# Kernel tuning notes

Measured on AMD Instinct MI355X. Metric: run time of the kernel, lower is better.

Reference implementation:

```python
import jax, jax.numpy as jnp
import numpy as np

NEG_INF = -1e9  # torch code uses masked_fill with -1e9, not -inf


def setup_inputs() -> dict:
    key = jax.random.key(0)
    ks = jax.random.split(key, 6)
    B, S, WL, D1, D2, OUT = 32, 128, 20, 300, 300, 300
    sequence = jax.random.normal(ks[0], (B, S, WL, D1), dtype=jnp.float32)
    vector = jax.random.normal(ks[1], (B, S, D2), dtype=jnp.float32)
    char_masks = jax.random.randint(ks[2], (B, S, WL), 0, 2, dtype=jnp.int32)
    W = jax.random.normal(ks[3], (OUT, D1 + D2), dtype=jnp.float32) * (1.0 / np.sqrt(D1 + D2))
    b = jax.random.normal(ks[4], (OUT,), dtype=jnp.float32) * 0.01
    v = jax.random.uniform(ks[5], (OUT,), dtype=jnp.float32, minval=-0.01, maxval=0.01)
    return {"sequence": sequence, "vector": vector, "char_masks": char_masks,
            "W": W, "b": b, "v": v}


def reference(sequence, vector, char_masks, W, b, v):
    # sequence: (B,S,WL,D1); vector: (B,S,D2); char_masks: (B,S,WL)
    D1 = sequence.shape[-1]
    # Linear on concat([sequence, vector_expanded]) == split matmul (avoids
    # materializing the (B,S,WL,D1+D2) concat):
    Ws, Wv = W[:, :D1], W[:, D1:]
    lin = (jnp.einsum('bswd,od->bswo', sequence, Ws)
           + jnp.einsum('bsd,od->bso', vector, Wv)[:, :, None, :]
           + b)                       # (B,S,WL,OUT)
    score = jnp.einsum('bswo,o->bsw', jnp.tanh(lin), v)  # (B,S,WL)
    score = jnp.where(char_masks == 0, NEG_INF, score)
    alphas = jax.nn.softmax(score, axis=2)               # over word_len
    weighted = jnp.einsum('bsw,bswd->bsd', alphas, sequence)  # (B,S,D1)
    return weighted
```

## Files before the change

### kernel.cpp

```cpp
#include <hip/hip_runtime.h>
#include <math.h>

#define NEG_INF -1000000000.0f

#define WL_  20
#define D1_  300
#define D2_  300
#define OUT_ 300
#define BS_  4096
#define PPB  2
#define NBLK (BS_ / PPB)
#define BM   40
#define MT   3
#define KS   10
#define FR   512
#define SLABS (MT * KS)

typedef __attribute__((ext_vector_type(8))) short bf16x8;
typedef __attribute__((ext_vector_type(8))) short short8v;
typedef __attribute__((ext_vector_type(4))) float f32x4;
typedef __attribute__((ext_vector_type(4))) unsigned int uint4v;

__device__ short g_Bpk[KS * 20 * FR];
__device__ short g_Wvpk[KS * 20 * FR];
__device__ float g_vlin[(size_t)BS_ * 320];

__device__ inline short f2bf(float f) {
    unsigned u = __float_as_uint(f);
    u += 0x7FFFu + ((u >> 16) & 1u);
    return (short)(u >> 16);
}
__device__ inline float bf2f(short s) {
    return __uint_as_float(((unsigned)(unsigned short)s) << 16);
}

__device__ inline void pack_store(short* Am, int s, int lane, float4 fa, float4 fb) {
    unsigned u0 = __float_as_uint(fa.x) + 0x8000u;
    unsigned u1 = __float_as_uint(fa.y) + 0x8000u;
    unsigned u2 = __float_as_uint(fa.z) + 0x8000u;
    unsigned u3 = __float_as_uint(fa.w) + 0x8000u;
    unsigned u4 = __float_as_uint(fb.x) + 0x8000u;
    unsigned u5 = __float_as_uint(fb.y) + 0x8000u;
    unsigned u6 = __float_as_uint(fb.z) + 0x8000u;
    unsigned u7 = __float_as_uint(fb.w) + 0x8000u;
    uint4v w;
    w.x = __builtin_amdgcn_perm(u1, u0, 0x07060302u);
    w.y = __builtin_amdgcn_perm(u3, u2, 0x07060302u);
    w.z = __builtin_amdgcn_perm(u5, u4, 0x07060302u);
    w.w = __builtin_amdgcn_perm(u7, u6, 0x07060302u);
    *(uint4v*)(Am + ((size_t)s * 64 + lane) * 8) = w;
}

#define GB (KS * 20 * 64)
#define GT2 (GB + GB)

__global__ __launch_bounds__(256) void prep_small(
    const float* __restrict__ W, const float* __restrict__ bias,
    short* Bpk, short* Wvpk)
{
    if (!Bpk) { Bpk = g_Bpk; Wvpk = g_Wvpk; }
    const int id = blockIdx.x * 256 + threadIdx.x;
    if (id >= GT2) return;
    short8v o8 = {0, 0, 0, 0, 0, 0, 0, 0};
    if (id < GB) {
        const int lane = id & 63, g = id >> 6;
        const int q = lane >> 4, l15 = lane & 15;
        const int ks = g / 20, tile = g % 20;
        const int o = tile * 16 + l15, k0 = ks * 32 + q * 8;
        if (o < OUT_) {
            #pragma unroll
            for (int e = 0; e < 8; ++e) {
                const int k = k0 + e;
                if (k < D1_) o8[e] = f2bf(W[(size_t)o * (D1_ + D2_) + k]);
            }
        }
        *(short8v*)(Bpk + (size_t)id * 8) = o8;
    } else {
        const int id4 = id - GB;
        const int lane = id4 & 63, g = id4 >> 6;
        const int q = lane >> 4, l15 = lane & 15;
        const int ks = g / 20, tile = g % 20;
        const int o = tile * 16 + l15, k0 = ks * 32 + q * 8;
        if (o < OUT_) {
            #pragma unroll
            for (int e = 0; e < 8; ++e) {
                const int k = k0 + e;
                if (k < D2_)        o8[e] = f2bf(W[(size_t)o * (D1_ + D2_) + D1_ + k]);
                else if (k == 319)  o8[e] = f2bf(bias[o]);
            }
        }
        *(short8v*)(Wvpk + (size_t)id4 * 8) = o8;
    }
}

__global__ __launch_bounds__(256) void vlin_direct(
    const float* __restrict__ vec, const short* Wvpk, float* vlin)
{
    if (!Wvpk) { Wvpk = g_Wvpk; vlin = g_vlin; }
    const int mtile = blockIdx.x;
    const int tid  = threadIdx.x;
    const int lane = tid & 63;
    const int wv   = tid >> 6;
    const int q = lane >> 4, l15 = lane & 15;

    const float* vp = vec + (size_t)(mtile * 16 + l15) * D2_;
    float4 ra[KS], rb[KS];
    #pragma unroll
    for (int ks = 0; ks < KS; ++ks) {
        const int k0 = ks * 32 + q * 8;
        float4 fa = {0.f, 0.f, 0.f, 0.f}, fb = {0.f, 0.f, 0.f, 0.f};
        if (k0 < 296) { fa = *(const float4*)(vp + k0); fb = *(const float4*)(vp + k0 + 4); }
        else if (k0 == 296) { fa = *(const float4*)(vp + k0); }
        ra[ks] = fa; rb[ks] = fb;
    }
    bf16x8 frag[KS];
    #pragma unroll
    for (int ks = 0; ks < KS; ++ks) {
        const int k0 = ks * 32 + q * 8;
        const float f[8] = {ra[ks].x, ra[ks].y, ra[ks].z, ra[ks].w,
                            rb[ks].x, rb[ks].y, rb[ks].z, rb[ks].w};
        short8v av = {0, 0, 0, 0, 0, 0, 0, 0};
        #pragma unroll
        for (int e = 0; e < 8; ++e) {
            const int k = k0 + e;
            if (k < D2_)       av[e] = f2bf(f[e]);
            else if (k == 319) av[e] = (short)0x3F80;
        }
        frag[ks] = (bf16x8)av;
    }

    f32x4 acc[5];
    #pragma unroll
    for (int j = 0; j < 5; ++j) acc[j] = {0.f, 0.f, 0.f, 0.f};
    const short* pwb = Wvpk + (size_t)(wv * 5) * FR + lane * 8;
    #pragma unroll
    for (int ks = 0; ks < KS; ++ks) {
        #pragma unroll
        for (int j = 0; j < 5; ++j) {
            const bf16x8 b = *(const bf16x8*)(pwb + j * FR);
            acc[j] = __builtin_amdgcn_mfma_f32_16x16x32_bf16(frag[ks], b, acc[j], 0, 0, 0);
        }
        pwb += 20 * FR;
    }
    const int row0 = mtile * 16 + q * 4;
    #pragma unroll
    for (int j = 0; j < 5; ++j)
        #pragma unroll
        for (int r = 0; r < 4; ++r)
            vlin[(size_t)(row0 + r) * 320 + (wv * 5 + j) * 16 + l15] = acc[j][r];
}

__global__ __launch_bounds__(256, 2) void attn_fused(
    const float* __restrict__ seq,
    const int*   __restrict__ masks,
    const float* __restrict__ vvec,
    const short* Bpk,
    const float* vlinbuf,
    float*       __restrict__ out)
{
    if (!Bpk) { Bpk = g_Bpk; vlinbuf = g_vlin; }

    __shared__ short Am[MT * KS * FR];
    __shared__ float sp[4][BM];
    __shared__ float alpha_lds[BM];

    const int tid  = threadIdx.x;
    const int lane = tid & 63;
    const int wv   = tid >> 6;
    const int q    = lane >> 4;
    const int l15  = lane & 15;
    const int blk  = blockIdx.x;

    {
        const float* sbase = seq + (size_t)blk * BM * D1_;
        float4 ra[8], rb[8];
        #pragma unroll
        for (int it = 0; it < 8; ++it) {
            const int s = wv + it * 4;
            float4 fa = {0.f, 0.f, 0.f, 0.f}, fb = {0.f, 0.f, 0.f, 0.f};
            if (s < SLABS) {
                const int tile = s / KS, ks = s % KS;
                const int row = tile * 16 + l15;
                const int k0 = ks * 32 + q * 8;
                if (row < BM) {
                    const float* p = sbase + (size_t)row * D1_ + k0;
                    if (k0 < 296) { fa = *(const float4*)p; fb = *(const float4*)(p + 4); }
                    else if (k0 == 296) { fa = *(const float4*)p; }
                }
            }
            ra[it] = fa; rb[it] = fb;
        }
        #pragma unroll
        for (int it = 0; it < 8; ++it) {
            const int s = wv + it * 4;
            if (s < SLABS) pack_store(Am, s, lane, ra[it], rb[it]);
        }
    }

    float vj[5];
    #pragma unroll
    for (int j = 0; j < 5; ++j) {
        const int col = wv * 80 + j * 16 + l15;
        vj[j] = (col < OUT_) ? vvec[col] : 0.f;
    }
    float vlp[PPB][5];
    #pragma unroll
    for (int p = 0; p < PPB; ++p)
        #pragma unroll
        for (int j = 0; j < 5; ++j)
            vlp[p][j] = vlinbuf[(size_t)(blk * PPB + p) * 320 + wv * 80 + j * 16 + l15];
    __syncthreads();

    f32x4 acc[MT][5];
    #pragma unroll
    for (int i = 0; i < MT; ++i)
        #pragma unroll
        for (int j = 0; j < 5; ++j) acc[i][j] = {0.f, 0.f, 0.f, 0.f};

    const short* pb[5];
    #pragma unroll
    for (int j = 0; j < 5; ++j)
        pb[j] = Bpk + (size_t)(wv * 5 + j) * FR + lane * 8;

    #pragma unroll
    for (int ks = 0; ks < KS; ++ks) {
        bf16x8 a[MT], b[5];
        #pragma unroll
        for (int i = 0; i < MT; ++i)
            a[i] = *(const bf16x8*)(Am + (((size_t)i * KS + ks) * 64 + lane) * 8);
        #pragma unroll
        for (int j = 0; j < 5; ++j)
            b[j] = *(const bf16x8*)(pb[j] + (size_t)ks * 20 * FR);
        #pragma unroll
        for (int i = 0; i < MT; ++i)
            #pragma unroll
            for (int j = 0; j < 5; ++j)
                acc[i][j] = __builtin_amdgcn_mfma_f32_16x16x32_bf16(a[i], b[j], acc[i][j], 0, 0, 0);
    }

    #pragma unroll
    for (int i = 0; i < MT; ++i) {
        #pragma unroll
        for (int r = 0; r < 4; ++r) {
            const int row = i * 16 + q * 4 + r;
            const bool hi = (row >= 20);
            float s = 0.f;
            #pragma unroll
            for (int j = 0; j < 5; ++j) {
                const float vlv = (i == 0) ? vlp[0][j]
                                : (i == 2) ? vlp[1][j]
                                : (hi ? vlp[1][j] : vlp[0][j]);
                const float x = acc[i][j][r] + vlv;
                const float e = __expf(2.f * x);
                s += (1.f - 2.f / (e + 1.f)) * vj[j];
            }
            s += __shfl_xor(s, 1, 64);
            s += __shfl_xor(s, 2, 64);
            s += __shfl_xor(s, 4, 64);
            s += __shfl_xor(s, 8, 64);
            if (l15 == 0 && row < BM) sp[wv][row] = s;
        }
    }
    __syncthreads();

    if (tid < PPB * 32) {
        const int p = tid >> 5;
        const int w = tid & 31;
        float s;
        if (w < WL_) {
            const int row = p * WL_ + w;
            const float sc = sp[0][row] + sp[1][row] + sp[2][row] + sp[3][row];
            const int mk = masks[(size_t)(blk * PPB + p) * WL_ + w];
            s = (mk == 0) ? NEG_INF : sc;
        } else {
            s = -INFINITY;
        }
        float m = s;
        #pragma unroll
        for (int off = 16; off; off >>= 1)
            m = fmaxf(m, __shfl_xor(m, off, 32));
        const float e = __expf(s - m);
        float sum = e;
        #pragma unroll
        for (int off = 16; off; off >>= 1)
            sum += __shfl_xor(sum, off, 32);
        if (w < WL_) alpha_lds[p * WL_ + w] = e / sum;
    }
    __syncthreads();

    if (tid < PPB * 38) {
        const int p = tid / 38, ch = tid % 38;
        const int ks2 = ch >> 2, q2 = ch & 3;
        const int wst = ch % WL_;
        float o8[8] = {0.f, 0.f, 0.f, 0.f, 0.f, 0.f, 0.f, 0.f};
        #pragma unroll
        for (int wi = 0; wi < WL_; ++wi) {
            int w = wst + wi; if (w >= WL_) w -= WL_;
            const int row = p * WL_ + w;
            const int tl = row >> 4, l = row & 15;
            const bf16x8 s8 = *(const bf16x8*)(Am + (((size_t)tl * KS + ks2) * 64 + q2 * 16 + l) * 8);
            const float a = alpha_lds[row];
            #pragma unroll
            for (int e2 = 0; e2 < 8; ++e2) o8[e2] += a * bf2f(s8[e2]);
        }
        const int d0 = ch * 8, gp = blk * PPB + p;
        float* dst = out + (size_t)gp * OUT_ + d0;
        if (d0 + 8 <= OUT_) {
            *(float4*)dst       = {o8[0], o8[1], o8[2], o8[3]};
            *(float4*)(dst + 4) = {o8[4], o8[5], o8[6], o8[7]};
        } else {
            *(float4*)dst = {o8[0], o8[1], o8[2], o8[3]};
        }
    }
}

extern "C" void kernel_launch(void* const* d_in, const int* in_sizes, int n_in,
                              void* d_out, int out_size, void* d_ws, size_t ws_size,
                              hipStream_t stream) {
    const float* seq   = (const float*)d_in[0];
    const float* vec   = (const float*)d_in[1];
    const int*   masks = (const int*)d_in[2];
    const float* W     = (const float*)d_in[3];
    const float* b     = (const float*)d_in[4];
    const float* v     = (const float*)d_in[5];
    float* out = (float*)d_out;

    constexpr size_t SZ_B = sizeof(short) * (size_t)KS * 20 * FR;
    constexpr size_t SZ_L = sizeof(float) * (size_t)BS_ * 320;
    constexpr size_t NEED = SZ_B * 2 + SZ_L;
    short *Bpk = nullptr, *Wvpk = nullptr;
    float *vlin = nullptr;
    if (d_ws && ws_size >= NEED) {
        char* p = (char*)d_ws;
        Bpk  = (short*)p; p += SZ_B;
        Wvpk = (short*)p; p += SZ_B;
        vlin = (float*)p;
    }

    prep_small<<<(GT2 + 255) / 256, 256, 0, stream>>>(W, b, Bpk, Wvpk);
    vlin_direct<<<256, 256, 0, stream>>>(vec, Wvpk, vlin);
    attn_fused<<<NBLK, 256, 0, stream>>>(seq, masks, v, Bpk, vlin, out);
}
```

Measured before the change: 197.8 us.

## Merge prep and vlin kernels; double-buffer sequence tiles in persistent attention blocks

The weight-packing and vector-linear kernels become one launch: the vlin blocks now read and convert the W2/bias slice straight from global memory instead of waiting on a packed copy. The attention kernel now processes four tiles per block. It double-buffers the packed sequence in LDS and prefetches the next tile's sequence, vlin values and masks into registers while the current tile computes. This aims to hide global load latency and cut one launch. In exchange it doubles LDS use, raises register pressure (which may lower occupancy), and runs a quarter as many blocks.

```diff
diff --git a/kernel.cpp b/kernel.cpp
--- a/kernel.cpp
+++ b/kernel.cpp
@@ -9,7 +9,8 @@
 #define OUT_ 300
 #define BS_  4096
 #define PPB  2
-#define NBLK (BS_ / PPB)
+#define TPB  4
+#define NBLKP (BS_ / (PPB * TPB))
 #define BM   40
 #define MT   3
 #define KS   10
@@ -22,7 +23,6 @@
 typedef __attribute__((ext_vector_type(4))) unsigned int uint4v;
 
 __device__ short g_Bpk[KS * 20 * FR];
-__device__ short g_Wvpk[KS * 20 * FR];
 __device__ float g_vlin[(size_t)BS_ * 320];
 
 __device__ inline short f2bf(float f) {
@@ -34,7 +34,7 @@
     return __uint_as_float(((unsigned)(unsigned short)s) << 16);
 }
 
-__device__ inline void pack_store(short* Am, int s, int lane, float4 fa, float4 fb) {
+__device__ inline void pack_store(short* dst, int s, int lane, float4 fa, float4 fb) {
     unsigned u0 = __float_as_uint(fa.x) + 0x8000u;
     unsigned u1 = __float_as_uint(fa.y) + 0x8000u;
     unsigned u2 = __float_as_uint(fa.z) + 0x8000u;
@@ -48,25 +48,30 @@
     w.y = __builtin_amdgcn_perm(u3, u2, 0x07060302u);
     w.z = __builtin_amdgcn_perm(u5, u4, 0x07060302u);
     w.w = __builtin_amdgcn_perm(u7, u6, 0x07060302u);
-    *(uint4v*)(Am + ((size_t)s * 64 + lane) * 8) = w;
+    *(uint4v*)(dst + ((size_t)s * 64 + lane) * 8) = w;
 }
 
 #define GB (KS * 20 * 64)
-#define GT2 (GB + GB)
-
-__global__ __launch_bounds__(256) void prep_small(
+#define PREP_BLKS ((GB + 255) / 256)
+#define VLIN_BLKS 256
+
+__global__ __launch_bounds__(256) void prep_and_vlin(
     const float* __restrict__ W, const float* __restrict__ bias,
-    short* Bpk, short* Wvpk)
+    const float* __restrict__ vec,
+    short* Bpk, float* vlin)
 {
-    if (!Bpk) { Bpk = g_Bpk; Wvpk = g_Wvpk; }
-    const int id = blockIdx.x * 256 + threadIdx.x;
-    if (id >= GT2) return;
-    short8v o8 = {0, 0, 0, 0, 0, 0, 0, 0};
-    if (id < GB) {
-        const int lane = id & 63, g = id >> 6;
-        const int q = lane >> 4, l15 = lane & 15;
+    if (!Bpk) { Bpk = g_Bpk; vlin = g_vlin; }
+    const int tid  = threadIdx.x;
+    const int lane = tid & 63;
+    const int q = lane >> 4, l15 = lane & 15;
+
+    if (blockIdx.x < PREP_BLKS) {
+        const int id = blockIdx.x * 256 + tid;
+        if (id >= GB) return;
+        const int g = id >> 6;
         const int ks = g / 20, tile = g % 20;
         const int o = tile * 16 + l15, k0 = ks * 32 + q * 8;
+        short8v o8 = {0, 0, 0, 0, 0, 0, 0, 0};
         if (o < OUT_) {
             #pragma unroll
             for (int e = 0; e < 8; ++e) {
@@ -75,33 +80,11 @@
             }
         }
         *(short8v*)(Bpk + (size_t)id * 8) = o8;
-    } else {
-        const int id4 = id - GB;
-        const int lane = id4 & 63, g = id4 >> 6;
-        const int q = lane >> 4, l15 = lane & 15;
-        const int ks = g / 20, tile = g % 20;
-        const int o = tile * 16 + l15, k0 = ks * 32 + q * 8;
-        if (o < OUT_) {
-            #pragma unroll
-            for (int e = 0; e < 8; ++e) {
-                const int k = k0 + e;
-                if (k < D2_)        o8[e] = f2bf(W[(size_t)o * (D1_ + D2_) + D1_ + k]);
-                else if (k == 319)  o8[e] = f2bf(bias[o]);
-            }
-        }
-        *(short8v*)(Wvpk + (size_t)id4 * 8) = o8;
-    }
-}
-
-__global__ __launch_bounds__(256) void vlin_direct(
-    const float* __restrict__ vec, const short* Wvpk, float* vlin)
-{
-    if (!Wvpk) { Wvpk = g_Wvpk; vlin = g_vlin; }
-    const int mtile = blockIdx.x;
-    const int tid  = threadIdx.x;
-    const int lane = tid & 63;
-    const int wv   = tid >> 6;
-    const int q = lane >> 4, l15 = lane & 15;
+        return;
+    }
+
+    const int mtile = blockIdx.x - PREP_BLKS;
+    const int wv = tid >> 6;
 
     const float* vp = vec + (size_t)(mtile * 16 + l15) * D2_;
     float4 ra[KS], rb[KS];
@@ -132,16 +115,46 @@
     f32x4 acc[5];
     #pragma unroll
     for (int j = 0; j < 5; ++j) acc[j] = {0.f, 0.f, 0.f, 0.f};
-    const short* pwb = Wvpk + (size_t)(wv * 5) * FR + lane * 8;
-    #pragma unroll
-    for (int ks = 0; ks < KS; ++ks) {
-        #pragma unroll
-        for (int j = 0; j < 5; ++j) {
-            const bf16x8 b = *(const bf16x8*)(pwb + j * FR);
-            acc[j] = __builtin_amdgcn_mfma_f32_16x16x32_bf16(frag[ks], b, acc[j], 0, 0, 0);
-        }
-        pwb += 20 * FR;
-    }
+
+    #pragma unroll
+    for (int j = 0; j < 5; ++j) {
+        const int jt = wv * 5 + j;
+        const int o = jt * 16 + l15;
+        float4 ba[KS], bb[KS];
+        float bv = 0.f;
+        if (o < OUT_) {
+            const float* wp = W + (size_t)o * (D1_ + D2_) + D1_;
+            #pragma unroll
+            for (int ks = 0; ks < KS; ++ks) {
+                const int k0 = ks * 32 + q * 8;
+                float4 fa = {0.f, 0.f, 0.f, 0.f}, fb = {0.f, 0.f, 0.f, 0.f};
+                if (k0 < 296) { fa = *(const float4*)(wp + k0); fb = *(const float4*)(wp + k0 + 4); }
+                else if (k0 == 296) { fa = *(const float4*)(wp + k0); }
+                ba[ks] = fa; bb[ks] = fb;
+            }
+            bv = bias[o];
+        } else {
+            #pragma unroll
+            for (int ks = 0; ks < KS; ++ks) {
+                ba[ks] = {0.f, 0.f, 0.f, 0.f}; bb[ks] = {0.f, 0.f, 0.f, 0.f};
+            }
+        }
+        #pragma unroll
+        for (int ks = 0; ks < KS; ++ks) {
+            const int k0 = ks * 32 + q * 8;
+            const float f[8] = {ba[ks].x, ba[ks].y, ba[ks].z, ba[ks].w,
+                                bb[ks].x, bb[ks].y, bb[ks].z, bb[ks].w};
+            short8v bvv = {0, 0, 0, 0, 0, 0, 0, 0};
+            #pragma unroll
+            for (int e = 0; e < 8; ++e) {
+                const int k = k0 + e;
+                if (k < D2_)       bvv[e] = f2bf(f[e]);
+                else if (k == 319) bvv[e] = f2bf(bv);
+            }
+            acc[j] = __builtin_amdgcn_mfma_f32_16x16x32_bf16(frag[ks], (bf16x8)bvv, acc[j], 0, 0, 0);
+        }
+    }
+
     const int row0 = mtile * 16 + q * 4;
     #pragma unroll
     for (int j = 0; j < 5; ++j)
@@ -160,7 +173,7 @@
 {
     if (!Bpk) { Bpk = g_Bpk; vlinbuf = g_vlin; }
 
-    __shared__ short Am[MT * KS * FR];
+    __shared__ short Am[2][SLABS * FR];
     __shared__ float sp[4][BM];
     __shared__ float alpha_lds[BM];
 
@@ -170,10 +183,14 @@
     const int q    = lane >> 4;
     const int l15  = lane & 15;
     const int blk  = blockIdx.x;
-
-    {
-        const float* sbase = seq + (size_t)blk * BM * D1_;
-        float4 ra[8], rb[8];
+    const int gt0  = blk * TPB;
+
+    float4 ra[8], rb[8];
+    float vlpc[PPB][5], vlpn[PPB][5];
+    int mkc = 0, mkn = 0;
+
+    auto issue_tile = [&](int gt) {
+        const float* sbase = seq + (size_t)gt * BM * D1_;
         #pragma unroll
         for (int it = 0; it < 8; ++it) {
             const int s = wv + it * 4;
@@ -191,11 +208,22 @@
             ra[it] = fa; rb[it] = fb;
         }
         #pragma unroll
+        for (int p = 0; p < PPB; ++p)
+            #pragma unroll
+            for (int j = 0; j < 5; ++j)
+                vlpn[p][j] = vlinbuf[(size_t)(gt * PPB + p) * 320 + wv * 80 + j * 16 + l15];
+        if (tid < PPB * 32) {
+            const int p = tid >> 5, w = tid & 31;
+            mkn = (w < WL_) ? masks[(size_t)(gt * PPB + p) * WL_ + w] : 0;
+        }
+    };
+    auto pack_tile = [&](short* dst) {
+        #pragma unroll
         for (int it = 0; it < 8; ++it) {
             const int s = wv + it * 4;
-            if (s < SLABS) pack_store(Am, s, lane, ra[it], rb[it]);
-        }
-    }
+            if (s < SLABS) pack_store(dst, s, lane, ra[it], rb[it]);
+        }
+    };
 
     float vj[5];
     #pragma unroll
@@ -203,113 +231,134 @@
         const int col = wv * 80 + j * 16 + l15;
         vj[j] = (col < OUT_) ? vvec[col] : 0.f;
     }
-    float vlp[PPB][5];
+
+    issue_tile(gt0);
+    pack_tile(&Am[0][0]);
     #pragma unroll
     for (int p = 0; p < PPB; ++p)
         #pragma unroll
-        for (int j = 0; j < 5; ++j)
-            vlp[p][j] = vlinbuf[(size_t)(blk * PPB + p) * 320 + wv * 80 + j * 16 + l15];
-    __syncthreads();
-
-    f32x4 acc[MT][5];
-    #pragma unroll
-    for (int i = 0; i < MT; ++i)
-        #pragma unroll
-        for (int j = 0; j < 5; ++j) acc[i][j] = {0.f, 0.f, 0.f, 0.f};
+        for (int j = 0; j < 5; ++j) vlpc[p][j] = vlpn[p][j];
+    mkc = mkn;
+    issue_tile(gt0 + 1);
+
+    short* cur = &Am[0][0];
+    short* nxt = &Am[1][0];
 
     const short* pb[5];
     #pragma unroll
     for (int j = 0; j < 5; ++j)
         pb[j] = Bpk + (size_t)(wv * 5 + j) * FR + lane * 8;
 
-    #pragma unroll
-    for (int ks = 0; ks < KS; ++ks) {
-        bf16x8 a[MT], b[5];
+    #pragma unroll 1
+    for (int t = 0; t < TPB; ++t) {
+        const int gt = gt0 + t;
+        __syncthreads();
+
+        f32x4 acc[MT][5];
         #pragma unroll
         for (int i = 0; i < MT; ++i)
-            a[i] = *(const bf16x8*)(Am + (((size_t)i * KS + ks) * 64 + lane) * 8);
-        #pragma unroll
-        for (int j = 0; j < 5; ++j)
-            b[j] = *(const bf16x8*)(pb[j] + (size_t)ks * 20 * FR);
-        #pragma unroll
-        for (int i = 0; i < MT; ++i)
+            #pragma unroll
+            for (int j = 0; j < 5; ++j) acc[i][j] = {0.f, 0.f, 0.f, 0.f};
+
+        #pragma unroll
+        for (int ks = 0; ks < KS; ++ks) {
+            bf16x8 a[MT], b[5];
+            #pragma unroll
+            for (int i = 0; i < MT; ++i)
+                a[i] = *(const bf16x8*)(cur + (((size_t)i * KS + ks) * 64 + lane) * 8);
             #pragma unroll
             for (int j = 0; j < 5; ++j)
-                acc[i][j] = __builtin_amdgcn_mfma_f32_16x16x32_bf16(a[i], b[j], acc[i][j], 0, 0, 0);
-    }
-
-    #pragma unroll
-    for (int i = 0; i < MT; ++i) {
-        #pragma unroll
-        for (int r = 0; r < 4; ++r) {
-            const int row = i * 16 + q * 4 + r;
-            const bool hi = (row >= 20);
-            float s = 0.f;
-            #pragma unroll
-            for (int j = 0; j < 5; ++j) {
-                const float vlv = (i == 0) ? vlp[0][j]
-                                : (i == 2) ? vlp[1][j]
-                                : (hi ? vlp[1][j] : vlp[0][j]);
-                const float x = acc[i][j][r] + vlv;
-                const float e = __expf(2.f * x);
-                s += (1.f - 2.f / (e + 1.f)) * vj[j];
-            }
-            s += __shfl_xor(s, 1, 64);
-            s += __shfl_xor(s, 2, 64);
-            s += __shfl_xor(s, 4, 64);
-            s += __shfl_xor(s, 8, 64);
-            if (l15 == 0 && row < BM) sp[wv][row] = s;
-        }
-    }
-    __syncthreads();
-
-    if (tid < PPB * 32) {
-        const int p = tid >> 5;
-        const int w = tid & 31;
-        float s;
-        if (w < WL_) {
-            const int row = p * WL_ + w;
-            const float sc = sp[0][row] + sp[1][row] + sp[2][row] + sp[3][row];
-            const int mk = masks[(size_t)(blk * PPB + p) * WL_ + w];
-            s = (mk == 0) ? NEG_INF : sc;
-        } else {
-            s = -INFINITY;
-        }
-        float m = s;
-        #pragma unroll
-        for (int off = 16; off; off >>= 1)
-            m = fmaxf(m, __shfl_xor(m, off, 32));
-        const float e = __expf(s - m);
-        float sum = e;
-        #pragma unroll
-        for (int off = 16; off; off >>= 1)
-            sum += __shfl_xor(sum, off, 32);
-        if (w < WL_) alpha_lds[p * WL_ + w] = e / sum;
-    }
-    __syncthreads();
-
-    if (tid < PPB * 38) {
-        const int p = tid / 38, ch = tid % 38;
-        const int ks2 = ch >> 2, q2 = ch & 3;
-        const int wst = ch % WL_;
-        float o8[8] = {0.f, 0.f, 0.f, 0.f, 0.f, 0.f, 0.f, 0.f};
-        #pragma unroll
-        for (int wi = 0; wi < WL_; ++wi) {
-            int w = wst + wi; if (w >= WL_) w -= WL_;
-            const int row = p * WL_ + w;
-            const int tl = row >> 4, l = row & 15;
-            const bf16x8 s8 = *(const bf16x8*)(Am + (((size_t)tl * KS + ks2) * 64 + q2 * 16 + l) * 8);
-            const float a = alpha_lds[row];
-            #pragma unroll
-            for (int e2 = 0; e2 < 8; ++e2) o8[e2] += a * bf2f(s8[e2]);
-        }
-        const int d0 = ch * 8, gp = blk * PPB + p;
-        float* dst = out + (size_t)gp * OUT_ + d0;
-        if (d0 + 8 <= OUT_) {
-            *(float4*)dst       = {o8[0], o8[1], o8[2], o8[3]};
-            *(float4*)(dst + 4) = {o8[4], o8[5], o8[6], o8[7]};
-        } else {
-            *(float4*)dst = {o8[0], o8[1], o8[2], o8[3]};
+                b[j] = *(const bf16x8*)(pb[j] + (size_t)ks * 20 * FR);
+            #pragma unroll
+            for (int i = 0; i < MT; ++i)
+                #pragma unroll
+                for (int j = 0; j < 5; ++j)
+                    acc[i][j] = __builtin_amdgcn_mfma_f32_16x16x32_bf16(a[i], b[j], acc[i][j], 0, 0, 0);
+        }
+
+        #pragma unroll
+        for (int i = 0; i < MT; ++i) {
+            #pragma unroll
+            for (int r = 0; r < 4; ++r) {
+                const int row = i * 16 + q * 4 + r;
+                const bool hi = (row >= 20);
+                float s = 0.f;
+                #pragma unroll
+                for (int j = 0; j < 5; ++j) {
+                    const float vlv = (i == 0) ? vlpc[0][j]
+                                    : (i == 2) ? vlpc[1][j]
+                                    : (hi ? vlpc[1][j] : vlpc[0][j]);
+                    const float x = acc[i][j][r] + vlv;
+                    const float e = __expf(2.f * x);
+                    s += (1.f - 2.f / (e + 1.f)) * vj[j];
+                }
+                s += __shfl_xor(s, 1, 64);
+                s += __shfl_xor(s, 2, 64);
+                s += __shfl_xor(s, 4, 64);
+                s += __shfl_xor(s, 8, 64);
+                if (l15 == 0 && row < BM) sp[wv][row] = s;
+            }
+        }
+        __syncthreads();
+
+        if (tid < PPB * 32) {
+            const int p = tid >> 5;
+            const int w = tid & 31;
+            float s;
+            if (w < WL_) {
+                const int row = p * WL_ + w;
+                const float sc = sp[0][row] + sp[1][row] + sp[2][row] + sp[3][row];
+                s = (mkc == 0) ? NEG_INF : sc;
+            } else {
+                s = -INFINITY;
+            }
+            float m = s;
+            #pragma unroll
+            for (int off = 16; off; off >>= 1)
+                m = fmaxf(m, __shfl_xor(m, off, 32));
+            const float e = __expf(s - m);
+            float sum = e;
+            #pragma unroll
+            for (int off = 16; off; off >>= 1)
+                sum += __shfl_xor(sum, off, 32);
+            if (w < WL_) alpha_lds[p * WL_ + w] = e / sum;
+        }
+        __syncthreads();
+
+        if (tid < PPB * 38) {
+            const int p = tid / 38, ch = tid % 38;
+            const int ks2 = ch >> 2, q2 = ch & 3;
+            const int wst = ch % WL_;
+            float o8[8] = {0.f, 0.f, 0.f, 0.f, 0.f, 0.f, 0.f, 0.f};
+            #pragma unroll
+            for (int wi = 0; wi < WL_; ++wi) {
+                int w = wst + wi; if (w >= WL_) w -= WL_;
+                const int row = p * WL_ + w;
+                const int tl = row >> 4, l = row & 15;
+                const bf16x8 s8 = *(const bf16x8*)(cur + (((size_t)tl * KS + ks2) * 64 + q2 * 16 + l) * 8);
+                const float a = alpha_lds[row];
+                #pragma unroll
+                for (int e2 = 0; e2 < 8; ++e2) o8[e2] += a * bf2f(s8[e2]);
+            }
+            const int d0 = ch * 8, gp = gt * PPB + p;
+            float* dst = out + (size_t)gp * OUT_ + d0;
+            if (d0 + 8 <= OUT_) {
+                *(float4*)dst       = {o8[0], o8[1], o8[2], o8[3]};
+                *(float4*)(dst + 4) = {o8[4], o8[5], o8[6], o8[7]};
+            } else {
+                *(float4*)dst = {o8[0], o8[1], o8[2], o8[3]};
+            }
+        }
+
+        if (t + 1 < TPB) {
+            pack_tile(nxt);
+            #pragma unroll
+            for (int p = 0; p < PPB; ++p)
+                #pragma unroll
+                for (int j = 0; j < 5; ++j) vlpc[p][j] = vlpn[p][j];
+            mkc = mkn;
+            if (t + 2 < TPB) issue_tile(gt0 + t + 2);
+            short* tmp = cur; cur = nxt; nxt = tmp;
         }
     }
 }
@@ -327,17 +376,15 @@
 
     constexpr size_t SZ_B = sizeof(short) * (size_t)KS * 20 * FR;
     constexpr size_t SZ_L = sizeof(float) * (size_t)BS_ * 320;
-    constexpr size_t NEED = SZ_B * 2 + SZ_L;
-    short *Bpk = nullptr, *Wvpk = nullptr;
+    constexpr size_t NEED = SZ_B + SZ_L;
+    short *Bpk = nullptr;
     float *vlin = nullptr;
     if (d_ws && ws_size >= NEED) {
         char* p = (char*)d_ws;
         Bpk  = (short*)p; p += SZ_B;
-        Wvpk = (short*)p; p += SZ_B;
         vlin = (float*)p;
     }
 
-    prep_small<<<(GT2 + 255) / 256, 256, 0, stream>>>(W, b, Bpk, Wvpk);
-    vlin_direct<<<256, 256, 0, stream>>>(vec, Wvpk, vlin);
-    attn_fused<<<NBLK, 256, 0, stream>>>(seq, masks, v, Bpk, vlin, out);
-}
+    prep_and_vlin<<<PREP_BLKS + VLIN_BLKS, 256, 0, stream>>>(W, b, vec, Bpk, vlin);
+    attn_fused<<<NBLKP, 256, 0, stream>>>(seq, masks, v, Bpk, vlin, out);
+}
```

After: 296.7 us. +50.0%, slower.
